# Kernel optimization log

Hardware: AMD Instinct MI355X
Metric: run time of the kernel (lower is better)

## Reference

```python
import jax, jax.numpy as jnp
import numpy as np
from functools import partial

T, B = 1000, 256
STATE_DIM, ACTION_DIM, REWARD_DIM = 64, 8, 1
EMBED = 64
HIDDEN = 256


def setup_inputs() -> dict:
    key = jax.random.key(0)
    ks = jax.random.split(key, 12)
    g = lambda k, shape, fan_in: jax.random.normal(k, shape, jnp.float32) * np.sqrt(2.0 / fan_in)
    return {
        "states": jax.random.normal(ks[0], (T, B, STATE_DIM), jnp.float32),
        "actions": jax.random.normal(ks[1], (T, B, ACTION_DIM), jnp.float32),
        "rewards": jax.random.normal(ks[2], (T, B, REWARD_DIM), jnp.float32),
        # embedding linears (VarianceScaling(2.0) init, zero bias)
        "Ws": g(ks[3], (STATE_DIM, EMBED), STATE_DIM), "bs": jnp.zeros((EMBED,), jnp.float32),
        "Wa": g(ks[4], (ACTION_DIM, EMBED), ACTION_DIM), "ba": jnp.zeros((EMBED,), jnp.float32),
        "Wr": g(ks[5], (REWARD_DIM, EMBED), REWARD_DIM), "br": jnp.zeros((EMBED,), jnp.float32),
        # hk.GRU params: w_i [in, 3H], w_h [H, 3H], b [3H]
        "wi": g(ks[6], (3 * EMBED, 3 * HIDDEN), 3 * EMBED),
        "wh": g(ks[7], (HIDDEN, 3 * HIDDEN), HIDDEN),
        "bg": jnp.zeros((3 * HIDDEN,), jnp.float32),
    }


def _gru_scan(x_seq, h0, wi, wh, bg):
    # x_seq: [T, B, 3*EMBED]; hk.GRU math: z,r = sigmoid gates; a = tanh candidate
    H = HIDDEN
    wh_zr, wh_a = wh[:, : 2 * H], wh[:, 2 * H :]
    b_zr, b_a = bg[: 2 * H], bg[2 * H :]

    def step(h, gx):  # gx = x @ wi precomputed, [B, 3H]
        zr = jax.nn.sigmoid(gx[:, : 2 * H] + h @ wh_zr + b_zr)
        z, r = zr[:, :H], zr[:, H:]
        a = jnp.tanh(gx[:, 2 * H :] + (r * h) @ wh_a + b_a)
        h_next = (1.0 - z) * h + z * a
        return h_next, h_next

    gx_seq = jnp.einsum("tbd,dh->tbh", x_seq, wi)  # one big matmul over all steps
    _, hs = jax.lax.scan(step, h0, gx_seq)
    return hs  # [T, B, H]


def reference(states, actions, rewards, Ws, bs, Wa, ba, Wr, br, wi, wh, bg):
    se = jax.nn.gelu(states @ Ws + bs)
    ae = jax.nn.gelu(actions @ Wa + ba)
    re = jax.nn.gelu(rewards @ Wr + br)
    x = jnp.concatenate((se, ae, re), axis=-1)  # [T, B, 3*EMBED]
    h0 = jnp.zeros((x.shape[1], HIDDEN), x.dtype)
    return _gru_scan(x, h0, wi, wh, bg)
```

## Files before the change

kernel.cpp:

```cpp
#include <hip/hip_runtime.h>
#include <hip/hip_bf16.h>

#define TT   1000
#define BB   256
#define HID  256
#define GD   768
#define XD   192
#define NROW (TT*BB)

typedef __attribute__((ext_vector_type(8))) _Float16 half8;
typedef __attribute__((ext_vector_type(4))) float    float4_t;
typedef __attribute__((ext_vector_type(2))) unsigned uint2_t;

#define MFMA16(A,B,C) __builtin_amdgcn_mfma_f32_16x16x32_f16((A),(B),(C),0,0,0)

__device__ __forceinline__ void gll16(const void* g, void* l) {
  __builtin_amdgcn_global_load_lds((const __attribute__((address_space(1))) void*)g,
                                   (__attribute__((address_space(3))) void*)l, 16, 0, 0);
}

__device__ __forceinline__ unsigned short f2h(float f) {
  _Float16 h = (_Float16)f;
  union { _Float16 h; unsigned short u; } c; c.h = h; return c.u;
}
__device__ __forceinline__ uint2_t pk4h(float4_t v) {
  union { _Float16 h[4]; uint2_t u; } c;
  c.h[0] = (_Float16)v.x; c.h[1] = (_Float16)v.y;
  c.h[2] = (_Float16)v.z; c.h[3] = (_Float16)v.w;
  return c.u;
}
__device__ __forceinline__ float4_t h4_to_f4(uint2_t v) {
  union { uint2_t u; _Float16 h[4]; } c; c.u = v;
  float4_t f;
  f.x = (float)c.h[0]; f.y = (float)c.h[1];
  f.z = (float)c.h[2]; f.w = (float)c.h[3];
  return f;
}
__device__ __forceinline__ float sigx(float x) {
  return __builtin_amdgcn_rcpf(1.0f + __builtin_amdgcn_exp2f(-1.4426950408889634f * x));
}
__device__ __forceinline__ float tanhx(float x) {
  return 1.0f - 2.0f * __builtin_amdgcn_rcpf(1.0f + __builtin_amdgcn_exp2f(2.8853900817779268f * x));
}
__device__ __forceinline__ float4_t sig4(float4_t v){ float4_t o; o.x=sigx(v.x); o.y=sigx(v.y); o.z=sigx(v.z); o.w=sigx(v.w); return o; }
__device__ __forceinline__ float4_t tanh4(float4_t v){ float4_t o; o.x=tanhx(v.x); o.y=tanhx(v.y); o.z=tanhx(v.z); o.w=tanhx(v.w); return o; }
__device__ __forceinline__ float gelu1(float v){
  float c = v + 0.044715f * v * v * v;
  float e = __builtin_amdgcn_exp2f((0.7978845608028654f * 2.8853900817779268f) * c);
  float th = 1.0f - 2.0f * __builtin_amdgcn_rcpf(1.0f + e);
  return 0.5f * v * (1.0f + th);
}

__global__ void k_prep(const float* __restrict__ wi, const float* __restrict__ wh,
                       unsigned short* __restrict__ wiT, unsigned short* __restrict__ whF)
{
  int tid = blockIdx.x * 256 + threadIdx.x;
  if (tid < GD*XD) {
    int n = tid / XD, k = tid - n*XD;
    wiT[tid] = f2h(wi[(size_t)k*GD + n]);
  }
  int t2 = tid - GD*XD;
  if (t2 >= 0 && t2 < 48*8*64*8) {
    int j = t2 & 7, l = (t2 >> 3) & 63, f = t2 >> 9;
    int mf = f >> 3, kf = f & 7;
    int k = kf*32 + ((l >> 4) << 3) + j;
    int n = (mf << 4) + (l & 15);
    whF[t2] = f2h(wh[(size_t)k*GD + n]);
  }
}

__global__ void k_embed(const float* __restrict__ st, const float* __restrict__ ac,
                        const float* __restrict__ rw,
                        const float* __restrict__ Ws, const float* __restrict__ bs,
                        const float* __restrict__ Wa, const float* __restrict__ ba,
                        const float* __restrict__ Wr, const float* __restrict__ br,
                        unsigned short* __restrict__ x)
{
  int lane = threadIdx.x & 63;
  int wid = blockIdx.x * (blockDim.x >> 6) + (threadIdx.x >> 6);
  int nw  = gridDim.x * (blockDim.x >> 6);
  float wsr[64], war[8];
  #pragma unroll
  for (int k = 0; k < 64; ++k) wsr[k] = Ws[k*64 + lane];
  #pragma unroll
  for (int k = 0; k < 8; ++k) war[k] = Wa[k*64 + lane];
  float wrr = Wr[lane];
  float bsv = bs[lane], bav = ba[lane], brv = br[lane];
  for (int row = wid; row < NROW; row += nw) {
    const float4_t* sp = (const float4_t*)(st + (size_t)row*64);
    float a0 = bsv;
    #pragma unroll
    for (int q = 0; q < 16; ++q) {
      float4_t v = sp[q];
      a0 = fmaf(v.x, wsr[4*q+0], a0);
      a0 = fmaf(v.y, wsr[4*q+1], a0);
      a0 = fmaf(v.z, wsr[4*q+2], a0);
      a0 = fmaf(v.w, wsr[4*q+3], a0);
    }
    const float4_t* ap = (const float4_t*)(ac + (size_t)row*8);
    float a1 = bav;
    #pragma unroll
    for (int q = 0; q < 2; ++q) {
      float4_t v = ap[q];
      a1 = fmaf(v.x, war[4*q+0], a1);
      a1 = fmaf(v.y, war[4*q+1], a1);
      a1 = fmaf(v.z, war[4*q+2], a1);
      a1 = fmaf(v.w, war[4*q+3], a1);
    }
    float a2 = fmaf(rw[row], wrr, brv);
    unsigned short* xr = x + (size_t)row*XD;
    xr[lane]       = f2h(gelu1(a0));
    xr[64 + lane]  = f2h(gelu1(a1));
    xr[128 + lane] = f2h(gelu1(a2));
  }
}

__global__ __launch_bounds__(512, 2) void k_gx(const unsigned short* __restrict__ x,
                                               const unsigned short* __restrict__ wiT,
                                               const float* __restrict__ bg,
                                               unsigned short* __restrict__ gx)
{
  __shared__ half8 Xs[24*64];
  __shared__ half8 As[16*64];
  int lane = threadIdx.x & 63;
  int wv   = threadIdx.x >> 6;
  int b    = lane & 15;
  int g8   = (lane >> 4) << 3;
  int row0 = blockIdx.x * 64;
  #pragma unroll
  for (int i = 0; i < 3; ++i) {
    int c = wv*3 + i, nf = c / 6, kf = c - nf*6;
    gll16(x + (size_t)(row0 + nf*16 + b)*XD + kf*32 + g8, &Xs[c*64]);
  }
  int g4 = g8 >> 1;
  float4_t acc[6][4];
  #pragma unroll
  for (int i = 0; i < 6; ++i) {
    float4_t bgv = *(const float4_t*)(bg + (wv + 8*i)*16 + g4);
    #pragma unroll
    for (int nf = 0; nf < 4; ++nf) acc[i][nf] = bgv;
  }
  half8 xb[4];
  for (int kf = 0; kf < 6; ++kf) {
    #pragma unroll
    for (int p = 0; p < 3; ++p) {
      __syncthreads();
      #pragma unroll
      for (int i2 = 0; i2 < 2; ++i2) {
        int q = wv*2 + i2;
        gll16(wiT + (size_t)((p*16 + q)*16 + b)*XD + kf*32 + g8, &As[q*64]);
      }
      __syncthreads();
      if (p == 0) {
        #pragma unroll
        for (int nf = 0; nf < 4; ++nf) xb[nf] = Xs[(nf*6 + kf)*64 + lane];
      }
      half8 af0 = As[wv*64 + lane];
      half8 af1 = As[(wv+8)*64 + lane];
      #pragma unroll
      for (int nf = 0; nf < 4; ++nf) {
        acc[2*p  ][nf] = MFMA16(af0, xb[nf], acc[2*p  ][nf]);
        acc[2*p+1][nf] = MFMA16(af1, xb[nf], acc[2*p+1][nf]);
      }
    }
  }
  #pragma unroll
  for (int i = 0; i < 6; ++i) {
    #pragma unroll
    for (int nf = 0; nf < 4; ++nf) {
      size_t idx = (size_t)(row0 + nf*16 + b)*GD + (wv + 8*i)*16 + g4;
      *(uint2_t*)(gx + idx) = pk4h(acc[i][nf]);
    }
  }
}

__global__
__attribute__((amdgpu_flat_work_group_size(512, 512), amdgpu_waves_per_eu(2, 2)))
void k_gru(const unsigned short* __restrict__ gx,
           const unsigned short* __restrict__ whF,
           float* __restrict__ out)
{
  __shared__ char smem[98304];
  char* h_lds  = smem;
  char* rh_lds = smem + 8192;
  char* gxb    = smem + 16384;
  const int tid  = threadIdx.x;
  const int lane = tid & 63;
  const int wv   = tid >> 6;
  const int wg   = blockIdx.x;
  const int b    = lane & 15;
  const int g    = lane >> 4;
  const int kr4  = g << 2;
  const int xm   = (b & 7) << 4;

  half8 wz0[8], wz1[8], wr0[8], wr1[8], wa0[8], wa1[8];
  #pragma unroll
  for (int kf = 0; kf < 8; ++kf) {
    wz0[kf] = *(const half8*)(whF + ((size_t)((( 2*wv    )*8 + kf)*64 + lane) << 3));
    wz1[kf] = *(const half8*)(whF + ((size_t)((( 2*wv + 1)*8 + kf)*64 + lane) << 3));
    wr0[kf] = *(const half8*)(whF + ((size_t)(((16 + 2*wv)*8 + kf)*64 + lane) << 3));
    wr1[kf] = *(const half8*)(whF + ((size_t)(((17 + 2*wv)*8 + kf)*64 + lane) << 3));
    wa0[kf] = *(const half8*)(whF + ((size_t)(((32 + 2*wv)*8 + kf)*64 + lane) << 3));
    wa1[kf] = *(const half8*)(whF + ((size_t)(((33 + 2*wv)*8 + kf)*64 + lane) << 3));
  }
  #pragma unroll
  for (int kf = 0; kf < 8; ++kf) {
    asm volatile("" : "+v"(wz0[kf]));
    asm volatile("" : "+v"(wz1[kf]));
    asm volatile("" : "+v"(wr0[kf]));
    asm volatile("" : "+v"(wr1[kf]));
    asm volatile("" : "+v"(wa0[kf]));
    asm volatile("" : "+v"(wa1[kf]));
  }
  for (int i = tid; i < 2048; i += 512) ((unsigned*)h_lds)[i] = 0u;

  int soff[3], dch[3];
  #pragma unroll
  for (int i = 0; i < 3; ++i) {
    int c = wv*3 + i;
    int doff = c*1024 + lane*16;
    int brow = doff / 1536;
    int cb = doff - brow*1536;
    soff[i] = brow*1536 + (cb ^ ((brow & 7) << 4));
    dch[i] = c*1024;
  }
  const char* gxc = (const char*)gx;
  #pragma unroll
  for (int i = 0; i < 3; ++i)
    gll16(gxc + (size_t)wg*24576 + soff[i], gxb + dch[i]);
  __syncthreads();

  float4_t hf0 = {0.f, 0.f, 0.f, 0.f}, hf1 = hf0;
  const char* hb_base = h_lds + b*512;
  const char* rb_base = rh_lds + b*512;
  const int off_z0 = ((wv*32      + kr4) << 1) ^ xm;
  const int off_z1 = ((wv*32 + 16 + kr4) << 1) ^ xm;

  for (int t = 0; t < TT; ++t) {
    asm volatile("s_waitcnt vmcnt(2) lgkmcnt(0)" ::: "memory");
    __builtin_amdgcn_s_barrier();
    asm volatile("" ::: "memory");
    if (t + 1 < TT) {
      const char* slab = gxc + (size_t)(t+1)*393216 + (size_t)wg*24576;
      char* dstb = gxb + 24576*((t+1) & 1);
      #pragma unroll
      for (int i = 0; i < 3; ++i) gll16(slab + soff[i], dstb + dch[i]);
    }
    const char* cur = gxb + 24576*(t & 1) + b*1536;
    float4_t az0 = h4_to_f4(*(const uint2_t*)(cur + off_z0));
    float4_t az1 = h4_to_f4(*(const uint2_t*)(cur + off_z1));
    float4_t ar0 = h4_to_f4(*(const uint2_t*)(cur + off_z0 + 512));
    float4_t ar1 = h4_to_f4(*(const uint2_t*)(cur + off_z1 + 512));
    #pragma unroll
    for (int kf = 0; kf < 8; ++kf) {
      half8 hb = *(const half8*)(hb_base + ((kf*64 + (g << 4)) ^ xm));
      az0 = MFMA16(wz0[kf], hb, az0);
      az1 = MFMA16(wz1[kf], hb, az1);
      ar0 = MFMA16(wr0[kf], hb, ar0);
      ar1 = MFMA16(wr1[kf], hb, ar1);
    }
    float4_t z0 = sig4(az0), z1 = sig4(az1);
    float4_t rh0 = sig4(ar0) * hf0, rh1 = sig4(ar1) * hf1;
    *(uint2_t*)(rh_lds + b*512 + off_z0) = pk4h(rh0);
    *(uint2_t*)(rh_lds + b*512 + off_z1) = pk4h(rh1);
    asm volatile("s_waitcnt lgkmcnt(0)" ::: "memory");
    __builtin_amdgcn_s_barrier();
    asm volatile("" ::: "memory");
    float4_t aa0 = h4_to_f4(*(const uint2_t*)(cur + off_z0 + 1024));
    float4_t aa1 = h4_to_f4(*(const uint2_t*)(cur + off_z1 + 1024));
    #pragma unroll
    for (int kf = 0; kf < 8; ++kf) {
      half8 rb = *(const half8*)(rb_base + ((kf*64 + (g << 4)) ^ xm));
      aa0 = MFMA16(wa0[kf], rb, aa0);
      aa1 = MFMA16(wa1[kf], rb, aa1);
    }
    float4_t a0 = tanh4(aa0), a1 = tanh4(aa1);
    float4_t hn0 = hf0 + z0 * (a0 - hf0);
    float4_t hn1 = hf1 + z1 * (a1 - hf1);
    hf0 = hn0; hf1 = hn1;
    *(uint2_t*)(h_lds + b*512 + off_z0) = pk4h(hn0);
    *(uint2_t*)(h_lds + b*512 + off_z1) = pk4h(hn1);
    float* op = out + (((size_t)t*BB + wg*16 + b) << 8) + wv*32 + kr4;
    *(float4_t*)op = hn0;
    *(float4_t*)(op + 16) = hn1;
  }
}

extern "C" void kernel_launch(void* const* d_in, const int* in_sizes, int n_in,
                              void* d_out, int out_size, void* d_ws, size_t ws_size,
                              hipStream_t stream) {
  (void)in_sizes; (void)n_in; (void)out_size; (void)ws_size;
  const float* states  = (const float*)d_in[0];
  const float* actions = (const float*)d_in[1];
  const float* rewards = (const float*)d_in[2];
  const float* Ws = (const float*)d_in[3];
  const float* bs = (const float*)d_in[4];
  const float* Wa = (const float*)d_in[5];
  const float* ba = (const float*)d_in[6];
  const float* Wr = (const float*)d_in[7];
  const float* br = (const float*)d_in[8];
  const float* wi = (const float*)d_in[9];
  const float* wh = (const float*)d_in[10];
  const float* bg = (const float*)d_in[11];
  char* wsb = (char*)d_ws;
  unsigned short* gx  = (unsigned short*)(wsb);
  unsigned short* x   = (unsigned short*)(wsb + 393216000LL);
  unsigned short* wiT = (unsigned short*)(wsb + 491520000LL);
  unsigned short* whF = (unsigned short*)(wsb + 491814912LL);
  k_prep <<<1344, 256, 0, stream>>>(wi, wh, wiT, whF);
  k_embed<<<1000, 256, 0, stream>>>(states, actions, rewards, Ws, bs, Wa, ba, Wr, br, x);
  k_gx   <<<4000, 512, 0, stream>>>(x, wiT, bg, gx);
  k_gru  <<<16, 512, 0, stream>>>(gx, whF, (float*)d_out);
}
```

Before: 2.273 ms.

## Store gx in MFMA fragment order and pad LDS rows instead of XOR swizzle

The input-projection kernel now writes gx directly in the per-lane MFMA accumulator fragment layout, grouped by (batch tile, gate block, nf), so the recurrent kernel can read each lane's gate preactivations with a flat lane*8 offset. The h and r*h LDS buffers switch from XOR swizzling to 528-byte padded rows to avoid bank conflicts with simpler addressing. This removes per-step swizzle arithmetic and makes the global-to-LDS prefetch contiguous, at the cost of slightly more LDS and a coupled layout contract between the two kernels.

```diff
diff --git a/kernel.cpp b/kernel.cpp
--- a/kernel.cpp
+++ b/kernel.cpp
@@ -164,12 +164,13 @@
       }
     }
   }
+  char* gxc = (char*)gx;
   #pragma unroll
   for (int i = 0; i < 6; ++i) {
     #pragma unroll
     for (int nf = 0; nf < 4; ++nf) {
-      size_t idx = (size_t)(row0 + nf*16 + b)*GD + (wv + 8*i)*16 + g4;
-      *(uint2_t*)(gx + idx) = pk4h(acc[i][nf]);
+      size_t idx = (((size_t)blockIdx.x*48 + (wv + 8*i))*4 + nf)*512 + lane*8;
+      *(uint2_t*)(gxc + idx) = pk4h(acc[i][nf]);
     }
   }
 }
@@ -182,8 +183,8 @@
 {
   __shared__ char smem[98304];
   char* h_lds  = smem;
-  char* rh_lds = smem + 8192;
-  char* gxb    = smem + 16384;
+  char* rh_lds = smem + 8448;
+  char* gxb    = smem + 16896;
   const int tid  = threadIdx.x;
   const int lane = tid & 63;
   const int wv   = tid >> 6;
@@ -191,7 +192,6 @@
   const int b    = lane & 15;
   const int g    = lane >> 4;
   const int kr4  = g << 2;
-  const int xm   = (b & 7) << 4;
 
   half8 wz0[8], wz1[8], wr0[8], wr1[8], wa0[8], wa1[8];
   #pragma unroll
@@ -212,48 +212,54 @@
     asm volatile("" : "+v"(wa0[kf]));
     asm volatile("" : "+v"(wa1[kf]));
   }
-  for (int i = tid; i < 2048; i += 512) ((unsigned*)h_lds)[i] = 0u;
-
+  for (int i = tid; i < 2112; i += 512) ((unsigned*)h_lds)[i] = 0u;
+
+  const int nf   = wg & 3;
+  const int bsel = wg >> 2;
   int soff[3], dch[3];
   #pragma unroll
   for (int i = 0; i < 3; ++i) {
-    int c = wv*3 + i;
-    int doff = c*1024 + lane*16;
-    int brow = doff / 1536;
-    int cb = doff - brow*1536;
-    soff[i] = brow*1536 + (cb ^ ((brow & 7) << 4));
-    dch[i] = c*1024;
+    int c = i*16 + (tid >> 5);
+    int r = (tid & 31) << 4;
+    soff[i] = nf*512 + c*2048 + r;
+    dch[i]  = i*8192 + tid*16;
   }
   const char* gxc = (const char*)gx;
   #pragma unroll
   for (int i = 0; i < 3; ++i)
-    gll16(gxc + (size_t)wg*24576 + soff[i], gxb + dch[i]);
+    gll16(gxc + (size_t)bsel*98304 + soff[i], gxb + dch[i]);
   __syncthreads();
 
   float4_t hf0 = {0.f, 0.f, 0.f, 0.f}, hf1 = hf0;
-  const char* hb_base = h_lds + b*512;
-  const char* rb_base = rh_lds + b*512;
-  const int off_z0 = ((wv*32      + kr4) << 1) ^ xm;
-  const int off_z1 = ((wv*32 + 16 + kr4) << 1) ^ xm;
+  const char* hb_base = h_lds + b*528;
+  const char* rb_base = rh_lds + b*528;
+  const int off_h0 = (wv*32 + kr4) << 1;
+  const int off_h1 = off_h0 + 32;
+  const int lz0 = ( 2*wv    )*512 + lane*8;
+  const int lz1 = ( 2*wv + 1)*512 + lane*8;
+  const int lr0 = (16 + 2*wv)*512 + lane*8;
+  const int lr1 = (17 + 2*wv)*512 + lane*8;
+  const int la0 = (32 + 2*wv)*512 + lane*8;
+  const int la1 = (33 + 2*wv)*512 + lane*8;
 
   for (int t = 0; t < TT; ++t) {
     asm volatile("s_waitcnt vmcnt(2) lgkmcnt(0)" ::: "memory");
     __builtin_amdgcn_s_barrier();
     asm volatile("" ::: "memory");
     if (t + 1 < TT) {
-      const char* slab = gxc + (size_t)(t+1)*393216 + (size_t)wg*24576;
+      const char* slab = gxc + ((size_t)(t+1)*4 + bsel)*98304;
       char* dstb = gxb + 24576*((t+1) & 1);
       #pragma unroll
       for (int i = 0; i < 3; ++i) gll16(slab + soff[i], dstb + dch[i]);
     }
-    const char* cur = gxb + 24576*(t & 1) + b*1536;
-    float4_t az0 = h4_to_f4(*(const uint2_t*)(cur + off_z0));
-    float4_t az1 = h4_to_f4(*(const uint2_t*)(cur + off_z1));
-    float4_t ar0 = h4_to_f4(*(const uint2_t*)(cur + off_z0 + 512));
-    float4_t ar1 = h4_to_f4(*(const uint2_t*)(cur + off_z1 + 512));
+    const char* cur = gxb + 24576*(t & 1);
+    float4_t az0 = h4_to_f4(*(const uint2_t*)(cur + lz0));
+    float4_t az1 = h4_to_f4(*(const uint2_t*)(cur + lz1));
+    float4_t ar0 = h4_to_f4(*(const uint2_t*)(cur + lr0));
+    float4_t ar1 = h4_to_f4(*(const uint2_t*)(cur + lr1));
     #pragma unroll
     for (int kf = 0; kf < 8; ++kf) {
-      half8 hb = *(const half8*)(hb_base + ((kf*64 + (g << 4)) ^ xm));
+      half8 hb = *(const half8*)(hb_base + kf*64 + (g << 4));
       az0 = MFMA16(wz0[kf], hb, az0);
       az1 = MFMA16(wz1[kf], hb, az1);
       ar0 = MFMA16(wr0[kf], hb, ar0);
@@ -261,16 +267,16 @@
     }
     float4_t z0 = sig4(az0), z1 = sig4(az1);
     float4_t rh0 = sig4(ar0) * hf0, rh1 = sig4(ar1) * hf1;
-    *(uint2_t*)(rh_lds + b*512 + off_z0) = pk4h(rh0);
-    *(uint2_t*)(rh_lds + b*512 + off_z1) = pk4h(rh1);
+    *(uint2_t*)(rh_lds + b*528 + off_h0) = pk4h(rh0);
+    *(uint2_t*)(rh_lds + b*528 + off_h1) = pk4h(rh1);
     asm volatile("s_waitcnt lgkmcnt(0)" ::: "memory");
     __builtin_amdgcn_s_barrier();
     asm volatile("" ::: "memory");
-    float4_t aa0 = h4_to_f4(*(const uint2_t*)(cur + off_z0 + 1024));
-    float4_t aa1 = h4_to_f4(*(const uint2_t*)(cur + off_z1 + 1024));
+    float4_t aa0 = h4_to_f4(*(const uint2_t*)(cur + la0));
+    float4_t aa1 = h4_to_f4(*(const uint2_t*)(cur + la1));
     #pragma unroll
     for (int kf = 0; kf < 8; ++kf) {
-      half8 rb = *(const half8*)(rb_base + ((kf*64 + (g << 4)) ^ xm));
+      half8 rb = *(const half8*)(rb_base + kf*64 + (g << 4));
       aa0 = MFMA16(wa0[kf], rb, aa0);
       aa1 = MFMA16(wa1[kf], rb, aa1);
     }
@@ -278,8 +284,8 @@
     float4_t hn0 = hf0 + z0 * (a0 - hf0);
     float4_t hn1 = hf1 + z1 * (a1 - hf1);
     hf0 = hn0; hf1 = hn1;
-    *(uint2_t*)(h_lds + b*512 + off_z0) = pk4h(hn0);
-    *(uint2_t*)(h_lds + b*512 + off_z1) = pk4h(hn1);
+    *(uint2_t*)(h_lds + b*528 + off_h0) = pk4h(hn0);
+    *(uint2_t*)(h_lds + b*528 + off_h1) = pk4h(hn1);
     float* op = out + (((size_t)t*BB + wg*16 + b) << 8) + wv*32 + kr4;
     *(float4_t*)op = hn0;
     *(float4_t*)(op + 16) = hn1;
```

Result: faster. 2.186 ms, median of 3 (-3.8%).
